# Optimization experiments

Hardware: AMD Instinct MI355X
Metric: run time of the kernel (lower is better)

## Reference

```python
import jax, jax.numpy as jnp
import numpy as np

# Structure constants C[i, j, k] for the Cl(3,0) geometric product with basis
# order [1, e1, e2, e3, e12, e13, e23, e123]: (a*b)_k = sum_ij a_i b_j C[i,j,k].
_TABLE = [
    (0,0,0,1),(1,1,0,1),(2,2,0,1),(3,3,0,1),(4,4,0,-1),(5,5,0,-1),(6,6,0,-1),(7,7,0,-1),
    (0,1,1,1),(1,0,1,1),(2,4,1,-1),(4,2,1,1),(3,5,1,-1),(5,3,1,1),(6,7,1,-1),(7,6,1,-1),
    (0,2,2,1),(2,0,2,1),(1,4,2,1),(4,1,2,-1),(3,6,2,-1),(6,3,2,1),(5,7,2,1),(7,5,2,1),
    (0,3,3,1),(3,0,3,1),(1,5,3,1),(5,1,3,-1),(2,6,3,1),(6,2,3,-1),(4,7,3,-1),(7,4,3,-1),
    (0,4,4,1),(4,0,4,1),(1,2,4,1),(2,1,4,-1),(3,7,4,1),(7,3,4,1),(5,6,4,-1),(6,5,4,1),
    (0,5,5,1),(5,0,5,1),(1,3,5,1),(3,1,5,-1),(2,7,5,-1),(7,2,5,-1),(4,6,5,1),(6,4,5,-1),
    (0,6,6,1),(6,0,6,1),(2,3,6,1),(3,2,6,-1),(1,7,6,1),(7,1,6,1),(4,5,6,-1),(5,4,6,1),
    (0,7,7,1),(7,0,7,1),(1,6,7,1),(6,1,7,1),(2,5,7,-1),(5,2,7,-1),(3,4,7,1),(4,3,7,1),
]
_C = np.zeros((8, 8, 8), dtype=np.float32)
for _i, _j, _k, _s in _TABLE:
    _C[_i, _j, _k] = _s

B, IN_F, OUT_F = 65536, 64, 64


def setup_inputs() -> dict:
    key = jax.random.key(0)
    ks = jax.random.split(key, 5)
    return {
        "x": jax.random.normal(ks[0], (B, IN_F, 8), dtype=jnp.float32),
        "weight": jax.random.normal(ks[1], (OUT_F, IN_F, 8), dtype=jnp.float32) * 0.02,
        "bias": jnp.zeros((OUT_F, 8), dtype=jnp.float32),
        "row_scale": jax.random.uniform(ks[2], (OUT_F,), dtype=jnp.float32),
        "col_scale": jax.random.uniform(ks[3], (IN_F,), dtype=jnp.float32),
        "bias_shift": jax.random.normal(ks[4], (OUT_F,), dtype=jnp.float32),
    }


def reference(x, weight, bias, row_scale, col_scale, bias_shift):
    C = jnp.asarray(_C)  # [8,8,8] structure constants
    w = weight * row_scale[:, None, None] * col_scale[None, :, None]
    w = jnp.nan_to_num(w, nan=0.0)
    # Fold structure constants into the (small) weight first: wc[o,n,i,k]
    wc = jnp.einsum('onj,ijk->onik', w, C)
    # out[b,o,k] = sum_{n,i} x[b,n,i] * wc[o,n,i,k]  (geometric product + sum over in)
    out = jnp.einsum('bni,onik->bok', x, wc)
    out = out + bias[None]
    out = out.at[..., 0].add(bias_shift[None, :])
    return out
```

## Files before the change

### kernel.cpp

```cpp
#include <hip/hip_runtime.h>
#include <cstdint>

#define M_DIM 65536
#define N_DIM 512
#define K_DIM 512
#define BM 128
#define BN 128
#define BK 32
#define KSTEPS (K_DIM / BK)

typedef float f32x4 __attribute__((ext_vector_type(4)));
typedef __bf16 bf16x8 __attribute__((ext_vector_type(8)));
typedef unsigned short us8 __attribute__((ext_vector_type(8)));

__device__ __forceinline__ unsigned short f2bf(float f) {
  unsigned int u = __builtin_bit_cast(unsigned int, f);
  u += 0x7fffu + ((u >> 16) & 1u);
  return (unsigned short)(u >> 16);
}

__device__ __forceinline__ void async_copy16(const void* gptr, void* ldsptr) {
  __builtin_amdgcn_global_load_lds(
      (const __attribute__((address_space(1))) void*)gptr,
      (__attribute__((address_space(3))) void*)ldsptr, 16, 0, 0);
}

__global__ void clifford_prep(const float* __restrict__ weight,
                              const float* __restrict__ bias,
                              const float* __restrict__ row_scale,
                              const float* __restrict__ col_scale,
                              const float* __restrict__ bias_shift,
                              unsigned short* __restrict__ WCT,
                              float* __restrict__ bias2) {
  const int t = blockIdx.x * 256 + threadIdx.x;
  if (t < 512) {
    const int o = t >> 3, k = t & 7;
    bias2[t] = bias[t] + (k == 0 ? bias_shift[o] : 0.0f);
  }
  if (t >= 64 * 64) return;
  const int o = t >> 6, n = t & 63;
  const float rs = row_scale[o], cs = col_scale[n];
  float w[8];
#pragma unroll
  for (int j = 0; j < 8; ++j) {
    float v = weight[(size_t)t * 8 + j] * rs * cs;
    w[j] = (v != v) ? 0.0f : v;
  }
  constexpr int TI[64] = {0,1,2,3,4,5,6,7, 0,1,2,4,3,5,6,7, 0,2,1,4,3,6,5,7,
                          0,3,1,5,2,6,4,7, 0,4,1,2,3,7,5,6, 0,5,1,3,2,7,4,6,
                          0,6,2,3,1,7,4,5, 0,7,1,6,2,5,3,4};
  constexpr int TJ[64] = {0,1,2,3,4,5,6,7, 1,0,4,2,5,3,7,6, 2,0,4,1,6,3,7,5,
                          3,0,5,1,6,2,7,4, 4,0,2,1,7,3,6,5, 5,0,3,1,7,2,6,4,
                          6,0,3,2,7,1,5,4, 7,0,6,1,5,2,4,3};
  constexpr int TK[64] = {0,0,0,0,0,0,0,0, 1,1,1,1,1,1,1,1, 2,2,2,2,2,2,2,2,
                          3,3,3,3,3,3,3,3, 4,4,4,4,4,4,4,4, 5,5,5,5,5,5,5,5,
                          6,6,6,6,6,6,6,6, 7,7,7,7,7,7,7,7};
  constexpr float TS[64] = {1,1,1,1,-1,-1,-1,-1, 1,1,-1,1,-1,1,-1,-1, 1,1,1,-1,-1,1,1,1,
                            1,1,1,-1,1,-1,-1,-1, 1,1,1,-1,1,1,-1,1,  1,1,1,-1,-1,-1,1,-1,
                            1,1,1,-1,1,1,-1,1,   1,1,1,1,-1,-1,1,1};
  float wc[8][8];
#pragma unroll
  for (int i = 0; i < 8; ++i)
#pragma unroll
    for (int k = 0; k < 8; ++k) wc[i][k] = 0.0f;
#pragma unroll
  for (int e = 0; e < 64; ++e) wc[TI[e]][TK[e]] += TS[e] * w[TJ[e]];
#pragma unroll
  for (int k = 0; k < 8; ++k)
#pragma unroll
    for (int i = 0; i < 8; ++i)
      WCT[(size_t)(o * 8 + k) * K_DIM + (n * 8 + i)] = f2bf(wc[i][k]);
}

__global__ __launch_bounds__(256) void clifford_gemm(
    const float* __restrict__ x, const unsigned short* __restrict__ WCT,
    const float* __restrict__ bias2, float* __restrict__ out) {
  __shared__ __align__(16) unsigned short As[2][BM * BK];
  __shared__ __align__(16) unsigned short Bs[2][BN * BK];

  const int tid = threadIdx.x;
  const int lane = tid & 63;
  const int wv = tid >> 6;

  const int bid = blockIdx.x;
  const int grp = bid >> 5, r = bid & 31;
  const size_t m0 = (size_t)(grp * 8 + (r & 7)) * BM;
  const int n0 = (r >> 3) * BN;

  const int s_row = tid >> 1;
  const int s_half = tid & 1;
  const float* ag = x + (m0 + s_row) * (size_t)K_DIM + s_half * 16;

  const int b_row = lane >> 2;
  const int b_grp = lane & 3;

  const int wm = (wv & 1) * 64;
  const int wn = (wv >> 1) * 64;
  const int lm = lane & 15;
  const int kg = lane >> 4;

  f32x4 ar[4];

  const f32x4 zero = {0.f, 0.f, 0.f, 0.f};
  f32x4 acc[4][4];
#pragma unroll
  for (int i = 0; i < 4; ++i)
#pragma unroll
    for (int j = 0; j < 4; ++j) acc[i][j] = zero;

  auto stageB = [&](int buf, int kc) {
    unsigned short* dst = &Bs[buf][(wv * 32) * BK];
#pragma unroll
    for (int ts = 0; ts < 2; ++ts) {
      const unsigned short* g =
          WCT + (size_t)(n0 + wv * 32 + ts * 16 + b_row) * K_DIM + kc + b_grp * 8;
      async_copy16(g, dst + ts * 16 * BK);
    }
  };
  auto loadA = [&](int kc) {
#pragma unroll
    for (int j = 0; j < 4; ++j) ar[j] = *(const f32x4*)(ag + kc + j * 4);
  };
  auto writeA = [&](int buf) {
    union { us8 v; unsigned short u[8]; } p0, p1;
#pragma unroll
    for (int j = 0; j < 4; ++j) {
      p0.u[j] = f2bf(ar[0][j]);
      p0.u[4 + j] = f2bf(ar[1][j]);
      p1.u[j] = f2bf(ar[2][j]);
      p1.u[4 + j] = f2bf(ar[3][j]);
    }
    unsigned short* dst = &As[buf][s_row * BK + s_half * 16];
    *(us8*)dst = p0.v;
    *(us8*)(dst + 8) = p1.v;
  };

  stageB(0, 0);
  loadA(0);
  writeA(0);
  __syncthreads();

  int buf = 0;
  for (int ks = 0; ks < KSTEPS; ++ks) {
    if (ks < KSTEPS - 1) {
      stageB(buf ^ 1, (ks + 1) * BK);
      loadA((ks + 1) * BK);
    }
    bf16x8 af[4], bfr[4];
#pragma unroll
    for (int mi = 0; mi < 4; ++mi)
      af[mi] = __builtin_bit_cast(
          bf16x8, *(const us8*)&As[buf][(wm + mi * 16 + lm) * BK + kg * 8]);
#pragma unroll
    for (int ni = 0; ni < 4; ++ni)
      bfr[ni] = __builtin_bit_cast(
          bf16x8, *(const us8*)&Bs[buf][(wn + ni * 16 + lm) * BK + kg * 8]);
#pragma unroll
    for (int mi = 0; mi < 4; ++mi)
#pragma unroll
      for (int ni = 0; ni < 4; ++ni)
        acc[mi][ni] = __builtin_amdgcn_mfma_f32_16x16x32_bf16(af[mi], bfr[ni],
                                                              acc[mi][ni], 0, 0, 0);
    if (ks < KSTEPS - 1) {
      writeA(buf ^ 1);
      __syncthreads();
      buf ^= 1;
    }
  }

#pragma unroll
  for (int ni = 0; ni < 4; ++ni) {
    const int nn = n0 + wn + ni * 16 + lm;
    const float b2 = bias2[nn];
#pragma unroll
    for (int mi = 0; mi < 4; ++mi) {
#pragma unroll
      for (int rr = 0; rr < 4; ++rr) {
        const size_t mm = m0 + wm + mi * 16 + kg * 4 + rr;
        out[mm * N_DIM + nn] = acc[mi][ni][rr] + b2;
      }
    }
  }
}

extern "C" void kernel_launch(void* const* d_in, const int* in_sizes, int n_in,
                              void* d_out, int out_size, void* d_ws, size_t ws_size,
                              hipStream_t stream) {
  const float* x          = (const float*)d_in[0];
  const float* weight     = (const float*)d_in[1];
  const float* bias       = (const float*)d_in[2];
  const float* row_scale  = (const float*)d_in[3];
  const float* col_scale  = (const float*)d_in[4];
  const float* bias_shift = (const float*)d_in[5];

  unsigned short* WCT = (unsigned short*)d_ws;
  float* bias2 = (float*)((char*)d_ws + (size_t)N_DIM * K_DIM * 2);

  clifford_prep<<<16, 256, 0, stream>>>(weight, bias, row_scale, col_scale,
                                        bias_shift, WCT, bias2);
  clifford_gemm<<<(M_DIM / BM) * (N_DIM / BN), 256, 0, stream>>>(
      x, WCT, bias2, (float*)d_out);
}
```

Baseline: 282.2 us.

## Load B fragments directly from pre-swizzled global layout, bypass LDS

The prep kernel now writes the folded weight in a fragment-friendly layout (k-group major, 8 contiguous bf16 per column), so each lane can load its MFMA B operand straight from global or L2 into registers, double-buffered across k-steps. This removes the B LDS staging and the reads back from it. The A tile's LDS layout also changes to k-group-major, and the fp32-to-bf16 conversion now uses the packed v_cvt_pk_bf16_f32 instruction. The cost is more register pressure from the B double buffers and many redundant global loads of B across waves and blocks, which now rely on cache hits.

```diff
diff --git a/kernel.cpp b/kernel.cpp
--- a/kernel.cpp
+++ b/kernel.cpp
@@ -19,10 +19,10 @@
   return (unsigned short)(u >> 16);
 }
 
-__device__ __forceinline__ void async_copy16(const void* gptr, void* ldsptr) {
-  __builtin_amdgcn_global_load_lds(
-      (const __attribute__((address_space(1))) void*)gptr,
-      (__attribute__((address_space(3))) void*)ldsptr, 16, 0, 0);
+__device__ __forceinline__ unsigned int cvt_pk_bf16(float lo, float hi) {
+  unsigned int r;
+  asm("v_cvt_pk_bf16_f32 %0, %1, %2" : "=v"(r) : "v"(lo), "v"(hi));
+  return r;
 }
 
 __global__ void clifford_prep(const float* __restrict__ weight,
@@ -30,7 +30,7 @@
                               const float* __restrict__ row_scale,
                               const float* __restrict__ col_scale,
                               const float* __restrict__ bias_shift,
-                              unsigned short* __restrict__ WCT,
+                              unsigned short* __restrict__ WCT2,
                               float* __restrict__ bias2) {
   const int t = blockIdx.x * 256 + threadIdx.x;
   if (t < 512) {
@@ -66,17 +66,16 @@
 #pragma unroll
   for (int e = 0; e < 64; ++e) wc[TI[e]][TK[e]] += TS[e] * w[TJ[e]];
 #pragma unroll
-  for (int k = 0; k < 8; ++k)
+  for (int kb = 0; kb < 8; ++kb)
 #pragma unroll
     for (int i = 0; i < 8; ++i)
-      WCT[(size_t)(o * 8 + k) * K_DIM + (n * 8 + i)] = f2bf(wc[i][k]);
+      WCT2[((size_t)n * N_DIM + o * 8 + kb) * 8 + i] = f2bf(wc[i][kb]);
 }
 
 __global__ __launch_bounds__(256) void clifford_gemm(
-    const float* __restrict__ x, const unsigned short* __restrict__ WCT,
+    const float* __restrict__ x, const unsigned short* __restrict__ WCT2,
     const float* __restrict__ bias2, float* __restrict__ out) {
   __shared__ __align__(16) unsigned short As[2][BM * BK];
-  __shared__ __align__(16) unsigned short Bs[2][BN * BK];
 
   const int tid = threadIdx.x;
   const int lane = tid & 63;
@@ -91,16 +90,14 @@
   const int s_half = tid & 1;
   const float* ag = x + (m0 + s_row) * (size_t)K_DIM + s_half * 16;
 
-  const int b_row = lane >> 2;
-  const int b_grp = lane & 3;
-
   const int wm = (wv & 1) * 64;
   const int wn = (wv >> 1) * 64;
   const int lm = lane & 15;
   const int kg = lane >> 4;
 
+  const unsigned short* bg = WCT2 + ((size_t)kg * N_DIM + (n0 + wn + lm)) * 8;
+
   f32x4 ar[4];
-
   const f32x4 zero = {0.f, 0.f, 0.f, 0.f};
   f32x4 acc[4][4];
 #pragma unroll
@@ -108,64 +105,64 @@
 #pragma unroll
     for (int j = 0; j < 4; ++j) acc[i][j] = zero;
 
-  auto stageB = [&](int buf, int kc) {
-    unsigned short* dst = &Bs[buf][(wv * 32) * BK];
-#pragma unroll
-    for (int ts = 0; ts < 2; ++ts) {
-      const unsigned short* g =
-          WCT + (size_t)(n0 + wv * 32 + ts * 16 + b_row) * K_DIM + kc + b_grp * 8;
-      async_copy16(g, dst + ts * 16 * BK);
-    }
-  };
   auto loadA = [&](int kc) {
 #pragma unroll
     for (int j = 0; j < 4; ++j) ar[j] = *(const f32x4*)(ag + kc + j * 4);
   };
-  auto writeA = [&](int buf) {
-    union { us8 v; unsigned short u[8]; } p0, p1;
-#pragma unroll
-    for (int j = 0; j < 4; ++j) {
-      p0.u[j] = f2bf(ar[0][j]);
-      p0.u[4 + j] = f2bf(ar[1][j]);
-      p1.u[j] = f2bf(ar[2][j]);
-      p1.u[4 + j] = f2bf(ar[3][j]);
-    }
-    unsigned short* dst = &As[buf][s_row * BK + s_half * 16];
-    *(us8*)dst = p0.v;
-    *(us8*)(dst + 8) = p1.v;
-  };
-
-  stageB(0, 0);
+  auto writeA = [&](int b) {
+    union { us8 v; unsigned int w[4]; } p0, p1;
+    p0.w[0] = cvt_pk_bf16(ar[0][0], ar[0][1]);
+    p0.w[1] = cvt_pk_bf16(ar[0][2], ar[0][3]);
+    p0.w[2] = cvt_pk_bf16(ar[1][0], ar[1][1]);
+    p0.w[3] = cvt_pk_bf16(ar[1][2], ar[1][3]);
+    p1.w[0] = cvt_pk_bf16(ar[2][0], ar[2][1]);
+    p1.w[1] = cvt_pk_bf16(ar[2][2], ar[2][3]);
+    p1.w[2] = cvt_pk_bf16(ar[3][0], ar[3][1]);
+    p1.w[3] = cvt_pk_bf16(ar[3][2], ar[3][3]);
+    unsigned short* d0 = &As[b][((s_half * 2) * BM + s_row) * 8];
+    unsigned short* d1 = &As[b][((s_half * 2 + 1) * BM + s_row) * 8];
+    *(us8*)d0 = p0.v;
+    *(us8*)d1 = p1.v;
+  };
+  auto loadB = [&](us8 (&bb)[4], int ks) {
+    const unsigned short* p = bg + (size_t)ks * (4 * N_DIM * 8);
+#pragma unroll
+    for (int ni = 0; ni < 4; ++ni) bb[ni] = *(const us8*)(p + ni * 128);
+  };
+
+  us8 b0[4], b1[4];
+
   loadA(0);
   writeA(0);
+  loadB(b0, 0);
   __syncthreads();
 
-  int buf = 0;
-  for (int ks = 0; ks < KSTEPS; ++ks) {
-    if (ks < KSTEPS - 1) {
-      stageB(buf ^ 1, (ks + 1) * BK);
+  auto body = [&](int ks, int pb, us8 (&bc)[4], us8 (&bn)[4]) {
+    const bool last = (ks == KSTEPS - 1);
+    if (!last) {
       loadA((ks + 1) * BK);
+      loadB(bn, ks + 1);
     }
-    bf16x8 af[4], bfr[4];
+    bf16x8 af[4];
 #pragma unroll
     for (int mi = 0; mi < 4; ++mi)
       af[mi] = __builtin_bit_cast(
-          bf16x8, *(const us8*)&As[buf][(wm + mi * 16 + lm) * BK + kg * 8]);
-#pragma unroll
-    for (int ni = 0; ni < 4; ++ni)
-      bfr[ni] = __builtin_bit_cast(
-          bf16x8, *(const us8*)&Bs[buf][(wn + ni * 16 + lm) * BK + kg * 8]);
+          bf16x8, *(const us8*)&As[pb][((size_t)kg * BM + wm + mi * 16 + lm) * 8]);
 #pragma unroll
     for (int mi = 0; mi < 4; ++mi)
 #pragma unroll
       for (int ni = 0; ni < 4; ++ni)
-        acc[mi][ni] = __builtin_amdgcn_mfma_f32_16x16x32_bf16(af[mi], bfr[ni],
-                                                              acc[mi][ni], 0, 0, 0);
-    if (ks < KSTEPS - 1) {
-      writeA(buf ^ 1);
+        acc[mi][ni] = __builtin_amdgcn_mfma_f32_16x16x32_bf16(
+            af[mi], __builtin_bit_cast(bf16x8, bc[ni]), acc[mi][ni], 0, 0, 0);
+    if (!last) {
+      writeA(pb ^ 1);
       __syncthreads();
-      buf ^= 1;
     }
+  };
+
+  for (int ks2 = 0; ks2 < KSTEPS; ks2 += 2) {
+    body(ks2, 0, b0, b1);
+    body(ks2 + 1, 1, b1, b0);
   }
 
 #pragma unroll
@@ -193,11 +190,11 @@
   const float* col_scale  = (const float*)d_in[4];
   const float* bias_shift = (const float*)d_in[5];
 
-  unsigned short* WCT = (unsigned short*)d_ws;
+  unsigned short* WCT2 = (unsigned short*)d_ws;
   float* bias2 = (float*)((char*)d_ws + (size_t)N_DIM * K_DIM * 2);
 
   clifford_prep<<<16, 256, 0, stream>>>(weight, bias, row_scale, col_scale,
-                                        bias_shift, WCT, bias2);
+                                        bias_shift, WCT2, bias2);
   clifford_gemm<<<(M_DIM / BM) * (N_DIM / BN), 256, 0, stream>>>(
-      x, WCT, bias2, (float*)d_out);
-}
+      x, WCT2, bias2, (float*)d_out);
+}
```

Result: no change. 283.7 us (+0.5%).
